# Performance work log

Hardware: AMD Instinct MI355X
Metric: run time of the kernel (lower is better)

The kernel has to match this reference:

```python
import jax, jax.numpy as jnp
import numpy as np

N, D, E = 100000, 32, 1600000
EH, NH = 32, 16
TAU = 0.1


def setup_inputs() -> dict:
    key = jax.random.key(0)
    ks = jax.random.split(key, 12)
    x = jax.random.normal(ks[0], (N, D), dtype=jnp.float32)
    edge_index = jax.random.randint(ks[1], (2, E), 0, N, dtype=jnp.int32)
    hsd = jax.random.normal(ks[2], (N,), dtype=jnp.float32)
    s_e1 = 1.0 / np.sqrt(D + 2)
    s_e2 = 1.0 / np.sqrt(EH)
    s_n2 = 1.0 / np.sqrt(NH)
    We1 = jax.random.uniform(ks[3], (D + 2, EH), jnp.float32, -s_e1, s_e1)
    be1 = jax.random.uniform(ks[4], (EH,), jnp.float32, -s_e1, s_e1)
    We2 = jax.random.uniform(ks[5], (EH, 1), jnp.float32, -s_e2, s_e2)
    be2 = jax.random.uniform(ks[6], (1,), jnp.float32, -s_e2, s_e2)
    Wn1 = jax.random.uniform(ks[7], (1, NH), jnp.float32, -1.0, 1.0)
    bn1 = jax.random.uniform(ks[8], (NH,), jnp.float32, -1.0, 1.0)
    Wn2 = jax.random.uniform(ks[9], (NH, 1), jnp.float32, -s_n2, s_n2)
    bn2 = jax.random.uniform(ks[10], (1,), jnp.float32, -s_n2, s_n2)
    return {"x": x, "hsd": hsd, "We1": We1, "be1": be1, "We2": We2, "be2": be2,
            "Wn1": Wn1, "bn1": bn1, "Wn2": Wn2, "bn2": bn2, "edge_index": edge_index}


def reference(x, hsd, We1, be1, We2, be2, Wn1, bn1, Wn2, bn2, edge_index):
    row, col = edge_index[0], edge_index[1]
    n = x.shape[0]
    # normalized HSD (torch.std is unbiased, ddof=1)
    hsd_norm = (hsd - hsd.mean()) / (jnp.std(hsd, ddof=1) + 1e-8)
    # edge MLP input: [hsd_u, hsd_v, |x_u - x_v|]  -> (E, D+2)
    diff_abs = jnp.abs(x[row] - x[col])
    edge_in = jnp.concatenate([hsd_norm[row][:, None], hsd_norm[col][:, None], diff_abs], axis=1)
    h = jax.nn.relu(edge_in @ We1 + be1)
    e_uv = (h @ We2 + be2)[:, 0]  # (E,)
    # segment softmax over destination (col)
    logits = e_uv / TAU
    seg_max = jax.ops.segment_max(logits, col, num_segments=n)
    seg_max = jnp.where(jnp.isfinite(seg_max), seg_max, 0.0)
    ex = jnp.exp(logits - seg_max[col])
    denom = jax.ops.segment_sum(ex, col, num_segments=n)
    alpha_uv = (ex / (denom[col] + 1e-16))[:, None]  # (E,1)
    # node-level gate
    gh = jax.nn.relu(hsd_norm[:, None] @ Wn1 + bn1)
    alpha_bar = jax.nn.sigmoid(gh @ Wn2 + bn2)  # (N,1)
    # degree normalization
    ones = jnp.ones(row.shape[0], dtype=x.dtype)
    src_deg = jnp.sqrt(jnp.clip(jax.ops.segment_sum(ones, row, num_segments=n), 1.0))
    dst_deg = jnp.sqrt(jnp.clip(jax.ops.segment_sum(ones, col, num_segments=n), 1.0))
    edge_w = 1.0 / (src_deg[row] * dst_deg[col])
    low_pass = jax.ops.segment_sum(edge_w[:, None] * x[row], col, num_segments=n)
    high_pass = jax.ops.segment_sum(alpha_uv * (x[col] - x[row]), col, num_segments=n)
    return (1.0 - alpha_bar) * low_pass + alpha_bar * high_pass
```

## Files before the change

kernel.cpp:

```cpp
#include <hip/hip_runtime.h>

#define D_FEAT 32
#define EHID 32
#define NHID 16
#define INV_TAU 10.0f
#define SCAN_CHUNK 1024
#define EPB 256
#define SDS 40
#define TILE 8192
#define BSH 7
#define NBIN 128
#define BMASK 127
#define CAP 3072

typedef __attribute__((ext_vector_type(8))) short short8v;
typedef __attribute__((ext_vector_type(4))) float f32x4;

__device__ __forceinline__ unsigned enc_f32(float f) {
    unsigned b = __float_as_uint(f);
    return (b & 0x80000000u) ? ~b : (b | 0x80000000u);
}
__device__ __forceinline__ float dec_f32(unsigned e) {
    unsigned b = (e & 0x80000000u) ? (e & 0x7fffffffu) : ~e;
    return __uint_as_float(b);
}
__device__ __forceinline__ unsigned short f2bf(float f) {
    unsigned u = __float_as_uint(f);
    u += 0x7fffu + ((u >> 16) & 1u);
    return (unsigned short)(u >> 16);
}
__device__ __forceinline__ float bflo(unsigned u) { return __uint_as_float(u << 16); }
__device__ __forceinline__ float bfhi(unsigned u) { return __uint_as_float(u & 0xFFFF0000u); }

__global__ __launch_bounds__(256) void kx_pack(const float* __restrict__ x,
                                               unsigned* __restrict__ xbf, int n2) {
    int i = blockIdx.x * 256 + threadIdx.x;
    if (i >= n2) return;
    float2 f = *(const float2*)(x + 2 * (size_t)i);
    xbf[i] = (unsigned)f2bf(f.x) | ((unsigned)f2bf(f.y) << 16);
}

__global__ __launch_bounds__(256) void k1_hsd_stats(const float* __restrict__ hsd,
                                                    double* __restrict__ stats, int N) {
    double s = 0.0, s2 = 0.0;
    for (int i = blockIdx.x * 256 + threadIdx.x; i < N; i += gridDim.x * 256) {
        double v = (double)hsd[i];
        s += v; s2 += v * v;
    }
    for (int off = 32; off > 0; off >>= 1) {
        s  += __shfl_down(s,  off, 64);
        s2 += __shfl_down(s2, off, 64);
    }
    __shared__ double ls[4], ls2[4];
    int wid = threadIdx.x >> 6, lid = threadIdx.x & 63;
    if (lid == 0) { ls[wid] = s; ls2[wid] = s2; }
    __syncthreads();
    if (threadIdx.x == 0) {
        double ts = 0.0, t2 = 0.0;
        for (int w = 0; w < 4; ++w) { ts += ls[w]; t2 += ls2[w]; }
        atomicAdd(stats, ts);
        atomicAdd(stats + 1, t2);
    }
}

__global__ __launch_bounds__(256) void k2_node_prep(const float* __restrict__ hsd,
                                                    const double* __restrict__ stats,
                                                    const float* __restrict__ Wn1,
                                                    const float* __restrict__ bn1,
                                                    const float* __restrict__ Wn2,
                                                    const float* __restrict__ bn2,
                                                    float* __restrict__ hsd_norm,
                                                    float* __restrict__ alpha_bar, int N) {
    int n = blockIdx.x * 256 + threadIdx.x;
    if (n >= N) return;
    double sum = stats[0], sumsq = stats[1];
    double mean = sum / (double)N;
    double var  = (sumsq - sum * sum / (double)N) / (double)(N - 1);
    float stdv  = (float)sqrt(var);
    float hn = (hsd[n] - (float)mean) / (stdv + 1e-8f);
    hsd_norm[n] = hn;
    float acc = bn2[0];
#pragma unroll
    for (int k = 0; k < NHID; ++k)
        acc += fmaxf(fmaf(hn, Wn1[k], bn1[k]), 0.0f) * Wn2[k];
    alpha_bar[n] = 1.0f / (1.0f + __expf(-acc));
}

__global__ __launch_bounds__(256) void s1_hist(const int* __restrict__ ei,
                                               int* __restrict__ hist,
                                               int E, int NB, int T, int M) {
    __shared__ int hv[1024], hu[1024];
    int t = threadIdx.x;
    for (int b = t; b < 1024; b += 256) { hv[b] = 0; hu[b] = 0; }
    __syncthreads();
    int base = blockIdx.x * TILE;
    for (int i = t; i < TILE; i += 256) {
        int e = base + i;
        if (e < E) {
            int u = ei[e], v = ei[E + e];
            atomicAdd(&hv[v >> BSH], 1);
            atomicAdd(&hu[u >> BSH], 1);
        }
    }
    __syncthreads();
    for (int b = t; b < NB; b += 256) {
        hist[b * T + blockIdx.x] = hv[b];
        hist[M + b * T + blockIdx.x] = hu[b];
    }
}

__global__ __launch_bounds__(256) void scan_k1(const int* __restrict__ cnt,
                                               int* __restrict__ out,
                                               int* __restrict__ partials, int N) {
    __shared__ int lds[256];
    int base = blockIdx.x * SCAN_CHUNK;
    int t = threadIdx.x;
    int v[4]; int loc = 0;
#pragma unroll
    for (int k = 0; k < 4; ++k) {
        int idx = base + t * 4 + k;
        v[k] = (idx < N) ? cnt[idx] : 0;
        loc += v[k];
    }
    lds[t] = loc; __syncthreads();
    for (int off = 1; off < 256; off <<= 1) {
        int a = (t >= off) ? lds[t - off] : 0;
        __syncthreads();
        lds[t] += a;
        __syncthreads();
    }
    int run = (t > 0) ? lds[t - 1] : 0;
    if (t == 255) partials[blockIdx.x] = lds[255];
#pragma unroll
    for (int k = 0; k < 4; ++k) {
        run += v[k];
        int idx = base + t * 4 + k;
        if (idx < N) out[idx + 1] = run;
    }
    if (blockIdx.x == 0 && t == 0) out[0] = 0;
}

__global__ __launch_bounds__(256) void scan_k2(int* __restrict__ partials, int B) {
    __shared__ int lds[256];
    int t = threadIdx.x;
    int v[4]; int loc = 0;
#pragma unroll
    for (int k = 0; k < 4; ++k) {
        int idx = t * 4 + k;
        v[k] = (idx < B) ? partials[idx] : 0;
        loc += v[k];
    }
    lds[t] = loc; __syncthreads();
    for (int off = 1; off < 256; off <<= 1) {
        int a = (t >= off) ? lds[t - off] : 0;
        __syncthreads();
        lds[t] += a;
        __syncthreads();
    }
    int run = (t > 0) ? lds[t - 1] : 0;
#pragma unroll
    for (int k = 0; k < 4; ++k) {
        int idx = t * 4 + k;
        if (idx < B) { partials[idx] = run; run += v[k]; }
    }
}

__global__ __launch_bounds__(256) void scan_k3(int* __restrict__ out,
                                               const int* __restrict__ partials, int N) {
    int i = blockIdx.x * 256 + threadIdx.x;
    if (i >= N) return;
    out[i + 1] += partials[i / SCAN_CHUNK];
}

__global__ __launch_bounds__(256) void s2_scatter(const int* __restrict__ ei,
                                                  const int* __restrict__ scanAll,
                                                  int2* __restrict__ coarse,
                                                  int* __restrict__ coarseU,
                                                  int E, int NB, int T, int M) {
    __shared__ int curV[1024], curU[1024];
    int t = threadIdx.x;
    for (int b = t; b < NB; b += 256) {
        curV[b] = scanAll[b * T + blockIdx.x];
        curU[b] = scanAll[M + b * T + blockIdx.x] - E;
    }
    __syncthreads();
    int base = blockIdx.x * TILE;
    for (int i = t; i < TILE; i += 256) {
        int e = base + i;
        if (e < E) {
            int u = ei[e], v = ei[E + e];
            int pv = atomicAdd(&curV[v >> BSH], 1);
            coarse[pv] = make_int2(u, v);
            int pu = atomicAdd(&curU[u >> BSH], 1);
            coarseU[pu] = u;
        }
    }
}

__global__ __launch_bounds__(256) void s3b_srccnt(const int* __restrict__ coarseU,
                                                  const int* __restrict__ scanAll,
                                                  float* __restrict__ inv_ssrc,
                                                  int N, int E, int NB, int T, int M) {
    __shared__ int cnt[NBIN];
    int t = threadIdx.x;
    int bin = blockIdx.x;
    int start = scanAll[M + bin * T] - E;
    int endv  = scanAll[M + (bin + 1) * T] - E;
    if (t < NBIN) cnt[t] = 0;
    __syncthreads();
    for (int i = start + t; i < endv; i += 256) atomicAdd(&cnt[coarseU[i] & BMASK], 1);
    __syncthreads();
    int vglob = (bin << BSH) + t;
    if (t < NBIN && vglob < N) inv_ssrc[vglob] = rsqrtf(fmaxf((float)cnt[t], 1.0f));
}

__global__ __launch_bounds__(256) void k3d_mlp(const unsigned* __restrict__ xbf,
                                               const float* __restrict__ hsd_norm,
                                               const float* __restrict__ We1,
                                               const float* __restrict__ be1,
                                               const float* __restrict__ We2,
                                               const float* __restrict__ be2,
                                               const int2* __restrict__ esorted,
                                               float* __restrict__ logit, int E) {
    __shared__ unsigned short sdiff[EPB * SDS];
    __shared__ unsigned short sB[4 * 64 * 8];

    int t = threadIdx.x;
    {
        int f = t >> 6, l = t & 63;
        int c = f >> 1, hh = f & 1;
        int col = hh * 16 + (l & 15);
        int k0 = c * 32 + (l >> 4) * 8;
        unsigned short vals[8];
#pragma unroll
        for (int b = 0; b < 8; ++b) {
            int k = k0 + b;
            int row = (k < 32) ? (k + 2) : (k == 32 ? 0 : (k == 33 ? 1 : -1));
            float w = (row >= 0) ? We1[row * EHID + col] : 0.0f;
            vals[b] = f2bf(w);
        }
        *(uint4*)&sB[(f * 64 + l) * 8] = *(const uint4*)vals;
    }

    int base = blockIdx.x * EPB;
    int q = t & 7;
#pragma unroll
    for (int k = 0; k < 8; ++k) {
        int s = (t >> 3) + 32 * k;
        int e = base + s;
        int ec = (e < E) ? e : (E - 1);
        int2 uv = esorted[ec];
        uint2 au = *(const uint2*)(xbf + (size_t)uv.x * 16 + q * 2);
        uint2 av = *(const uint2*)(xbf + (size_t)uv.y * 16 + q * 2);
        ushort4 pk;
        pk.x = f2bf(fabsf(bflo(au.x) - bflo(av.x)));
        pk.y = f2bf(fabsf(bfhi(au.x) - bfhi(av.x)));
        pk.z = f2bf(fabsf(bflo(au.y) - bflo(av.y)));
        pk.w = f2bf(fabsf(bfhi(au.y) - bfhi(av.y)));
        *(ushort4*)&sdiff[s * SDS + 4 * q] = pk;
        if (q == 0) {
            uint4 z;
            z.x = (unsigned)f2bf(hsd_norm[uv.x]) | ((unsigned)f2bf(hsd_norm[uv.y]) << 16);
            z.y = 0u; z.z = 0u; z.w = 0u;
            *(uint4*)&sdiff[s * SDS + 32] = z;
        }
    }
    __syncthreads();

    int l = t & 63, w = t >> 6;
    short8v B00 = *(const short8v*)&sB[(0 * 64 + l) * 8];
    short8v B01 = *(const short8v*)&sB[(1 * 64 + l) * 8];
    short8v B10 = *(const short8v*)&sB[(2 * 64 + l) * 8];
    short8v B11 = *(const short8v*)&sB[(3 * 64 + l) * 8];
    float blo = be1[l & 15], bhi = be1[16 + (l & 15)];
    float w2lo = We2[l & 15], w2hi = We2[16 + (l & 15)];
    float b2 = be2[0];
    int wbase = base + w * 64;

#pragma unroll
    for (int g = 0; g < 4; ++g) {
        int row = g * 16 + (l & 15) + w * 64;
        const short8v a0 = *(const short8v*)&sdiff[row * SDS + (l >> 4) * 8];
        short8v a1 = (short8v)(short)0;
        if (l < 16) a1 = *(const short8v*)&sdiff[row * SDS + 32];
        f32x4 c0 = {blo, blo, blo, blo};
        f32x4 c1 = {bhi, bhi, bhi, bhi};
        c0 = __builtin_amdgcn_mfma_f32_16x16x32_bf16(a0, B00, c0, 0, 0, 0);
        c0 = __builtin_amdgcn_mfma_f32_16x16x32_bf16(a1, B10, c0, 0, 0, 0);
        c1 = __builtin_amdgcn_mfma_f32_16x16x32_bf16(a0, B01, c1, 0, 0, 0);
        c1 = __builtin_amdgcn_mfma_f32_16x16x32_bf16(a1, B11, c1, 0, 0, 0);
#pragma unroll
        for (int r = 0; r < 4; ++r) {
            float vsum = fmaxf(c0[r], 0.0f) * w2lo + fmaxf(c1[r], 0.0f) * w2hi;
            vsum += __shfl_xor(vsum, 1, 64);
            vsum += __shfl_xor(vsum, 2, 64);
            vsum += __shfl_xor(vsum, 4, 64);
            vsum += __shfl_xor(vsum, 8, 64);
            int eo = wbase + g * 16 + (l >> 4) * 4 + r;
            if ((l & 15) == r && eo < E) logit[eo] = (vsum + b2) * INV_TAU;
        }
    }
}

__global__ __launch_bounds__(512) void k6a_tab(const int2* __restrict__ coarse,
                                               const float* __restrict__ logit,
                                               const int* __restrict__ scanAll,
                                               const float* __restrict__ inv_ssrc,
                                               const float* __restrict__ alpha_bar,
                                               int* __restrict__ usrc,
                                               float* __restrict__ coefG,
                                               int* __restrict__ dst_off,
                                               float* __restrict__ selfc,
                                               int N, int E, int NB, int T) {
    __shared__ int      su[CAP];
    __shared__ float    slg[CAP];
    __shared__ int      cnt[NBIN];
    __shared__ unsigned mEnc[NBIN];
    __shared__ float    den[NBIN], cA[NBIN], cB[NBIN];
    __shared__ int      base_[NBIN], cur_[NBIN];

    int t = threadIdx.x;
    int bin = blockIdx.x;
    int start = scanAll[bin * T];
    int n = scanAll[(bin + 1) * T] - start;
    if (n > CAP) n = CAP;

    if (t < NBIN) { cnt[t] = 0; mEnc[t] = 0u; den[t] = 0.0f; }
    __syncthreads();

    for (int i = t; i < n; i += 512) {
        int2 c = coarse[start + i];
        float lgv = logit[start + i];
        int vl = c.y & BMASK;
        su[i] = c.x | (vl << 17);
        slg[i] = lgv;
        atomicAdd(&cnt[vl], 1);
        atomicMax(&mEnc[vl], enc_f32(lgv));
    }
    __syncthreads();

    for (int i = t; i < n; i += 512) {
        int vl = su[i] >> 17;
        atomicAdd(&den[vl], __expf(slg[i] - dec_f32(mEnc[vl])));
    }
    __syncthreads();

    for (int off = 1; off < NBIN; off <<= 1) {
        int a = 0;
        if (t < NBIN && t >= off) a = cnt[t - off];
        __syncthreads();
        if (t < NBIN) cnt[t] += a;
        __syncthreads();
    }
    if (t < NBIN) {
        int b0 = (t > 0) ? cnt[t - 1] : 0;
        base_[t] = b0; cur_[t] = b0;
        int vg = (bin << BSH) + t;
        if (vg < N) {
            float ab = alpha_bar[vg];
            float d = den[t];
            float inv_den = 1.0f / (d + 1e-16f);
            int deg = cnt[t] - b0;
            cA[t] = -ab * inv_den;
            cB[t] = (1.0f - ab) * rsqrtf(fmaxf((float)deg, 1.0f));
            dst_off[vg] = start + b0;
            selfc[vg] = ab * (d * inv_den);
        }
    }
    if (bin == 0 && t == 0) dst_off[N] = E;
    __syncthreads();

    for (int i = t; i < n; i += 512) {
        int up = su[i];
        int vl = up >> 17;
        int u = up & 0x1FFFF;
        int p = start + atomicAdd(&cur_[vl], 1);
        float coef = fmaf(cA[vl], __expf(slg[i] - dec_f32(mEnc[vl])), cB[vl] * inv_ssrc[u]);
        usrc[p] = u;
        coefG[p] = coef;
    }
}

__global__ __launch_bounds__(256) void k7_gather(const unsigned* __restrict__ xbf,
                                                 const int* __restrict__ dst_off,
                                                 const int* __restrict__ usrc,
                                                 const float* __restrict__ coefG,
                                                 const float* __restrict__ selfc,
                                                 float* __restrict__ out, int N) {
    int v = blockIdx.x * 16 + (threadIdx.x >> 4);
    if (v >= N) return;
    int l = threadIdx.x & 15;

    int beg = dst_off[v], end = dst_off[v + 1];

    float a0 = 0.0f, a1 = 0.0f;
    int j = beg;
    for (; j + 3 < end; j += 4) {
        int u0 = usrc[j], u1 = usrc[j + 1], u2 = usrc[j + 2], u3 = usrc[j + 3];
        float c0 = coefG[j], c1 = coefG[j + 1], c2 = coefG[j + 2], c3 = coefG[j + 3];
        unsigned q0 = xbf[(size_t)u0 * 16 + l];
        unsigned q1 = xbf[(size_t)u1 * 16 + l];
        unsigned q2 = xbf[(size_t)u2 * 16 + l];
        unsigned q3 = xbf[(size_t)u3 * 16 + l];
        a0 = fmaf(c0, bflo(q0), a0); a1 = fmaf(c0, bfhi(q0), a1);
        a0 = fmaf(c1, bflo(q1), a0); a1 = fmaf(c1, bfhi(q1), a1);
        a0 = fmaf(c2, bflo(q2), a0); a1 = fmaf(c2, bfhi(q2), a1);
        a0 = fmaf(c3, bflo(q3), a0); a1 = fmaf(c3, bfhi(q3), a1);
    }
    for (; j < end; ++j) {
        unsigned q0 = xbf[(size_t)usrc[j] * 16 + l];
        float c0 = coefG[j];
        a0 = fmaf(c0, bflo(q0), a0); a1 = fmaf(c0, bfhi(q0), a1);
    }
    float sc = selfc[v];
    unsigned qv = xbf[(size_t)v * 16 + l];
    a0 = fmaf(sc, bflo(qv), a0);
    a1 = fmaf(sc, bfhi(qv), a1);
    float2 r; r.x = a0; r.y = a1;
    *(float2*)(out + (size_t)v * D_FEAT + 2 * l) = r;
}

extern "C" void kernel_launch(void* const* d_in, const int* in_sizes, int n_in,
                              void* d_out, int out_size, void* d_ws, size_t ws_size,
                              hipStream_t stream) {
    const float* x    = (const float*)d_in[0];
    const float* hsd  = (const float*)d_in[1];
    const float* We1  = (const float*)d_in[2];
    const float* be1  = (const float*)d_in[3];
    const float* We2  = (const float*)d_in[4];
    const float* be2  = (const float*)d_in[5];
    const float* Wn1  = (const float*)d_in[6];
    const float* bn1  = (const float*)d_in[7];
    const float* Wn2  = (const float*)d_in[8];
    const float* bn2  = (const float*)d_in[9];
    const int*   ei   = (const int*)d_in[10];
    float* out = (float*)d_out;

    const int N = in_sizes[1];
    const int E = in_sizes[10] / 2;
    const int NB = (N + NBIN - 1) >> BSH;
    const int T  = (E + TILE - 1) / TILE;
    const int M  = NB * T;
    const int M2 = 2 * M;

    char* ws = (char*)d_ws;
    size_t o = 0;
    auto alloc = [&](size_t bytes) { size_t r = o; o += (bytes + 255) & ~(size_t)255; return r; };
    double* stats     = (double*)(ws + alloc(16));
    float*  inv_ssrc  = (float*)(ws + alloc((size_t)4 * N));
    float*  hsd_norm  = (float*)(ws + alloc((size_t)4 * N));
    float*  alpha_bar = (float*)(ws + alloc((size_t)4 * N));
    float*  selfc     = (float*)(ws + alloc((size_t)4 * N));
    int*    dst_off   = (int*)(ws + alloc((size_t)4 * (N + 1)));
    int*    partials  = (int*)(ws + alloc(4096));
    int*    bufH      = (int*)(ws + alloc((size_t)4 * M2));
    int*    bufS      = (int*)(ws + alloc((size_t)4 * (M2 + 1)));
    int2*   coarse    = (int2*)(ws + alloc((size_t)8 * E));
    int*    coarseU   = (int*)(ws + alloc((size_t)4 * E));
    float*  logit     = (float*)(ws + alloc((size_t)4 * E));
    int*    usrc      = (int*)(ws + alloc((size_t)4 * E));
    float*  coefG     = (float*)(ws + alloc((size_t)4 * E));
    unsigned* xbf     = (unsigned*)coarseU;

    hipMemsetAsync(d_ws, 0, 256, stream);

    k1_hsd_stats<<<256, 256, 0, stream>>>(hsd, stats, N);
    k2_node_prep<<<(N + 255) / 256, 256, 0, stream>>>(hsd, stats, Wn1, bn1, Wn2, bn2,
                                                      hsd_norm, alpha_bar, N);

    s1_hist<<<T, 256, 0, stream>>>(ei, bufH, E, NB, T, M);

    int Bs = (M2 + SCAN_CHUNK - 1) / SCAN_CHUNK;
    scan_k1<<<Bs, 256, 0, stream>>>(bufH, bufS, partials, M2);
    scan_k2<<<1, 256, 0, stream>>>(partials, Bs);
    scan_k3<<<(M2 + 255) / 256, 256, 0, stream>>>(bufS, partials, M2);

    s2_scatter<<<T, 256, 0, stream>>>(ei, bufS, coarse, coarseU, E, NB, T, M);
    s3b_srccnt<<<NB, 256, 0, stream>>>(coarseU, bufS, inv_ssrc, N, E, NB, T, M);
    kx_pack<<<(N * (D_FEAT / 2) + 255) / 256, 256, 0, stream>>>(x, xbf, N * (D_FEAT / 2));
    k3d_mlp<<<(E + EPB - 1) / EPB, 256, 0, stream>>>(xbf, hsd_norm, We1, be1, We2, be2,
                                                     coarse, logit, E);
    k6a_tab<<<NB, 512, 0, stream>>>(coarse, logit, bufS, inv_ssrc, alpha_bar,
                                    usrc, coefG, dst_off, selfc, N, E, NB, T);
    k7_gather<<<(N + 15) / 16, 256, 0, stream>>>(xbf, dst_off, usrc, coefG, selfc, out, N);
}
```

Measured before the change: 288.6 us.

## Transpose edge-MLP MFMA so edges are columns and unroll gather by 8

```diff
diff --git a/kernel.cpp b/kernel.cpp
--- a/kernel.cpp
+++ b/kernel.cpp
@@ -6,7 +6,8 @@
 #define INV_TAU 10.0f
 #define SCAN_CHUNK 1024
 #define EPB 256
-#define SDS 40
+#define TPAD 272
+#define TILE_B (4 * TPAD)
 #define TILE 8192
 #define BSH 7
 #define NBIN 128
@@ -31,6 +32,11 @@
 }
 __device__ __forceinline__ float bflo(unsigned u) { return __uint_as_float(u << 16); }
 __device__ __forceinline__ float bfhi(unsigned u) { return __uint_as_float(u & 0xFFFF0000u); }
+__device__ __forceinline__ unsigned pkdiff(unsigned a, unsigned b) {
+    float d0 = fabsf(bflo(a) - bflo(b));
+    float d1 = fabsf(bfhi(a) - bfhi(b));
+    return (unsigned)f2bf(d0) | ((unsigned)f2bf(d1) << 16);
+}
 
 __global__ __launch_bounds__(256) void kx_pack(const float* __restrict__ x,
                                                unsigned* __restrict__ xbf, int n2) {
@@ -214,7 +220,7 @@
     if (t < NBIN && vglob < N) inv_ssrc[vglob] = rsqrtf(fmaxf((float)cnt[t], 1.0f));
 }
 
-__global__ __launch_bounds__(256) void k3d_mlp(const unsigned* __restrict__ xbf,
+__global__ __launch_bounds__(256) void k3e_mlp(const unsigned* __restrict__ xbf,
                                                const float* __restrict__ hsd_norm,
                                                const float* __restrict__ We1,
                                                const float* __restrict__ be1,
@@ -222,83 +228,79 @@
                                                const float* __restrict__ be2,
                                                const int2* __restrict__ esorted,
                                                float* __restrict__ logit, int E) {
-    __shared__ unsigned short sdiff[EPB * SDS];
-    __shared__ unsigned short sB[4 * 64 * 8];
-
-    int t = threadIdx.x;
-    {
-        int f = t >> 6, l = t & 63;
-        int c = f >> 1, hh = f & 1;
-        int col = hh * 16 + (l & 15);
-        int k0 = c * 32 + (l >> 4) * 8;
-        unsigned short vals[8];
-#pragma unroll
-        for (int b = 0; b < 8; ++b) {
-            int k = k0 + b;
-            int row = (k < 32) ? (k + 2) : (k == 32 ? 0 : (k == 33 ? 1 : -1));
-            float w = (row >= 0) ? We1[row * EHID + col] : 0.0f;
-            vals[b] = f2bf(w);
-        }
-        *(uint4*)&sB[(f * 64 + l) * 8] = *(const uint4*)vals;
-    }
-
+    __shared__ uint4 sdiff4[16 * TILE_B / 16];
+    __shared__ unsigned sh[EPB];
+    char* sdiff = (char*)sdiff4;
+
+    int t = threadIdx.x;
     int base = blockIdx.x * EPB;
-    int q = t & 7;
-#pragma unroll
-    for (int k = 0; k < 8; ++k) {
-        int s = (t >> 3) + 32 * k;
+    int l = t & 63, w = t >> 6;
+    int hq = l >> 4, hr = l & 15;
+
+    int q = t & 3;
+#pragma unroll
+    for (int p = 0; p < 4; ++p) {
+        int s = (t >> 2) + 64 * p;
         int e = base + s;
-        int ec = (e < E) ? e : (E - 1);
-        int2 uv = esorted[ec];
-        uint2 au = *(const uint2*)(xbf + (size_t)uv.x * 16 + q * 2);
-        uint2 av = *(const uint2*)(xbf + (size_t)uv.y * 16 + q * 2);
-        ushort4 pk;
-        pk.x = f2bf(fabsf(bflo(au.x) - bflo(av.x)));
-        pk.y = f2bf(fabsf(bfhi(au.x) - bfhi(av.x)));
-        pk.z = f2bf(fabsf(bflo(au.y) - bflo(av.y)));
-        pk.w = f2bf(fabsf(bfhi(au.y) - bfhi(av.y)));
-        *(ushort4*)&sdiff[s * SDS + 4 * q] = pk;
-        if (q == 0) {
-            uint4 z;
-            z.x = (unsigned)f2bf(hsd_norm[uv.x]) | ((unsigned)f2bf(hsd_norm[uv.y]) << 16);
-            z.y = 0u; z.z = 0u; z.w = 0u;
-            *(uint4*)&sdiff[s * SDS + 32] = z;
-        }
-    }
-    __syncthreads();
-
-    int l = t & 63, w = t >> 6;
-    short8v B00 = *(const short8v*)&sB[(0 * 64 + l) * 8];
-    short8v B01 = *(const short8v*)&sB[(1 * 64 + l) * 8];
-    short8v B10 = *(const short8v*)&sB[(2 * 64 + l) * 8];
-    short8v B11 = *(const short8v*)&sB[(3 * 64 + l) * 8];
-    float blo = be1[l & 15], bhi = be1[16 + (l & 15)];
-    float w2lo = We2[l & 15], w2hi = We2[16 + (l & 15)];
+        int2 uv = esorted[(e < E) ? e : (E - 1)];
+        uint4 au = *(const uint4*)(xbf + (size_t)uv.x * 16 + q * 4);
+        uint4 av = *(const uint4*)(xbf + (size_t)uv.y * 16 + q * 4);
+        uint4 outv;
+        outv.x = pkdiff(au.x, av.x);
+        outv.y = pkdiff(au.y, av.y);
+        outv.z = pkdiff(au.z, av.z);
+        outv.w = pkdiff(au.w, av.w);
+        *(uint4*)(sdiff + (s >> 4) * TILE_B + q * TPAD + (s & 15) * 16) = outv;
+        if (q == 0)
+            sh[s] = (unsigned)f2bf(hsd_norm[uv.x]) |
+                    ((unsigned)f2bf(hsd_norm[uv.y]) << 16);
+    }
+
+    unsigned short aw0[8], aw1[8];
+#pragma unroll
+    for (int b = 0; b < 8; ++b) {
+        aw0[b] = f2bf(We1[(hq * 8 + b + 2) * EHID + hr]);
+        aw1[b] = f2bf(We1[(hq * 8 + b + 2) * EHID + 16 + hr]);
+    }
+    short8v A0 = *(const short8v*)aw0;
+    short8v A1 = *(const short8v*)aw1;
+    float W0a[4], W1a[4], bea[4], W2a[4], W0b[4], W1b[4], beb[4], W2b[4];
+#pragma unroll
+    for (int r = 0; r < 4; ++r) {
+        int h = hq * 4 + r;
+        W0a[r] = We1[h];        W1a[r] = We1[EHID + h];
+        bea[r] = be1[h];        W2a[r] = We2[h];
+        int h2 = h + 16;
+        W0b[r] = We1[h2];       W1b[r] = We1[EHID + h2];
+        beb[r] = be1[h2];       W2b[r] = We2[h2];
+    }
     float b2 = be2[0];
-    int wbase = base + w * 64;
-
-#pragma unroll
-    for (int g = 0; g < 4; ++g) {
-        int row = g * 16 + (l & 15) + w * 64;
-        const short8v a0 = *(const short8v*)&sdiff[row * SDS + (l >> 4) * 8];
-        short8v a1 = (short8v)(short)0;
-        if (l < 16) a1 = *(const short8v*)&sdiff[row * SDS + 32];
-        f32x4 c0 = {blo, blo, blo, blo};
-        f32x4 c1 = {bhi, bhi, bhi, bhi};
-        c0 = __builtin_amdgcn_mfma_f32_16x16x32_bf16(a0, B00, c0, 0, 0, 0);
-        c0 = __builtin_amdgcn_mfma_f32_16x16x32_bf16(a1, B10, c0, 0, 0, 0);
-        c1 = __builtin_amdgcn_mfma_f32_16x16x32_bf16(a0, B01, c1, 0, 0, 0);
-        c1 = __builtin_amdgcn_mfma_f32_16x16x32_bf16(a1, B11, c1, 0, 0, 0);
+    __syncthreads();
+
+#pragma unroll
+    for (int gi = 0; gi < 4; ++gi) {
+        int g = w * 4 + gi;
+        short8v Bf = *(const short8v*)(sdiff + g * TILE_B + hq * TPAD + hr * 16);
+        unsigned hp = sh[g * 16 + hr];
+        float hu = bflo(hp), hv = bfhi(hp);
+        f32x4 c0, c1;
 #pragma unroll
         for (int r = 0; r < 4; ++r) {
-            float vsum = fmaxf(c0[r], 0.0f) * w2lo + fmaxf(c1[r], 0.0f) * w2hi;
-            vsum += __shfl_xor(vsum, 1, 64);
-            vsum += __shfl_xor(vsum, 2, 64);
-            vsum += __shfl_xor(vsum, 4, 64);
-            vsum += __shfl_xor(vsum, 8, 64);
-            int eo = wbase + g * 16 + (l >> 4) * 4 + r;
-            if ((l & 15) == r && eo < E) logit[eo] = (vsum + b2) * INV_TAU;
-        }
+            c0[r] = fmaf(hv, W1a[r], fmaf(hu, W0a[r], bea[r]));
+            c1[r] = fmaf(hv, W1b[r], fmaf(hu, W0b[r], beb[r]));
+        }
+        c0 = __builtin_amdgcn_mfma_f32_16x16x32_bf16(A0, Bf, c0, 0, 0, 0);
+        c1 = __builtin_amdgcn_mfma_f32_16x16x32_bf16(A1, Bf, c1, 0, 0, 0);
+        float vs = 0.0f;
+#pragma unroll
+        for (int r = 0; r < 4; ++r) {
+            vs = fmaf(fmaxf(c0[r], 0.0f), W2a[r], vs);
+            vs = fmaf(fmaxf(c1[r], 0.0f), W2b[r], vs);
+        }
+        vs += __shfl_xor(vs, 16, 64);
+        vs += __shfl_xor(vs, 32, 64);
+        int eo = base + g * 16 + hr;
+        if (hq == 0 && eo < E) logit[eo] = (vs + b2) * INV_TAU;
     }
 }
 
@@ -395,17 +397,17 @@
 
     float a0 = 0.0f, a1 = 0.0f;
     int j = beg;
-    for (; j + 3 < end; j += 4) {
-        int u0 = usrc[j], u1 = usrc[j + 1], u2 = usrc[j + 2], u3 = usrc[j + 3];
-        float c0 = coefG[j], c1 = coefG[j + 1], c2 = coefG[j + 2], c3 = coefG[j + 3];
-        unsigned q0 = xbf[(size_t)u0 * 16 + l];
-        unsigned q1 = xbf[(size_t)u1 * 16 + l];
-        unsigned q2 = xbf[(size_t)u2 * 16 + l];
-        unsigned q3 = xbf[(size_t)u3 * 16 + l];
-        a0 = fmaf(c0, bflo(q0), a0); a1 = fmaf(c0, bfhi(q0), a1);
-        a0 = fmaf(c1, bflo(q1), a0); a1 = fmaf(c1, bfhi(q1), a1);
-        a0 = fmaf(c2, bflo(q2), a0); a1 = fmaf(c2, bfhi(q2), a1);
-        a0 = fmaf(c3, bflo(q3), a0); a1 = fmaf(c3, bfhi(q3), a1);
+    for (; j + 7 < end; j += 8) {
+        int u_[8]; float c_[8]; unsigned q_[8];
+#pragma unroll
+        for (int k = 0; k < 8; ++k) { u_[k] = usrc[j + k]; c_[k] = coefG[j + k]; }
+#pragma unroll
+        for (int k = 0; k < 8; ++k) q_[k] = xbf[(size_t)u_[k] * 16 + l];
+#pragma unroll
+        for (int k = 0; k < 8; ++k) {
+            a0 = fmaf(c_[k], bflo(q_[k]), a0);
+            a1 = fmaf(c_[k], bfhi(q_[k]), a1);
+        }
     }
     for (; j < end; ++j) {
         unsigned q0 = xbf[(size_t)usrc[j] * 16 + l];
@@ -478,7 +480,7 @@
     s2_scatter<<<T, 256, 0, stream>>>(ei, bufS, coarse, coarseU, E, NB, T, M);
     s3b_srccnt<<<NB, 256, 0, stream>>>(coarseU, bufS, inv_ssrc, N, E, NB, T, M);
     kx_pack<<<(N * (D_FEAT / 2) + 255) / 256, 256, 0, stream>>>(x, xbf, N * (D_FEAT / 2));
-    k3d_mlp<<<(E + EPB - 1) / EPB, 256, 0, stream>>>(xbf, hsd_norm, We1, be1, We2, be2,
+    k3e_mlp<<<(E + EPB - 1) / EPB, 256, 0, stream>>>(xbf, hsd_norm, We1, be1, We2, be2,
                                                      coarse, logit, E);
     k6a_tab<<<NB, 512, 0, stream>>>(coarse, logit, bufS, inv_ssrc, alpha_bar,
                                     usrc, coefG, dst_off, selfc, N, E, NB, T);
```

Measured after the change: 269.8 us. 6.5% less time.
